# Kernel tuning notes

Measured on AMD Instinct MI355X. Metric: run time of the kernel, lower is better.

The kernel has to match this reference:

```python
import jax, jax.numpy as jnp
import numpy as np

B, S, MSL, MQL = 512, 20, 32, 16
E, H, HQ = 32, 32, 32
V, A = 10000, 1000
D = H + S  # per-object feature dim (hidden + one-hot tag) = 52
G = 256


def _lstm_last_h(x, Wih, Whh, bih, bhh):
    # x: [N, T, E]; torch LSTM gate order i,f,g,o; returns final hidden [N, H]
    n, t, _ = x.shape
    h_dim = Whh.shape[1]
    xp = jnp.einsum('nte,ge->ntg', x, Wih) + bih + bhh  # precompute input projection

    def step(carry, xt):
        h, c = carry
        gates = xt + h @ Whh.T
        i, f, g, o = jnp.split(gates, 4, axis=-1)
        c = jax.nn.sigmoid(f) * c + jax.nn.sigmoid(i) * jnp.tanh(g)
        h = jax.nn.sigmoid(o) * jnp.tanh(c)
        return (h, c), None

    init = (jnp.zeros((n, h_dim), x.dtype), jnp.zeros((n, h_dim), x.dtype))
    (h, _), _ = jax.lax.scan(step, init, xp.transpose(1, 0, 2))
    return h


def setup_inputs() -> dict:
    key = jax.random.key(0)
    ks = jax.random.split(key, 24)
    nrm = lambda k, shp, std=0.1: (jax.random.normal(k, shp) * std).astype(jnp.float32)
    inp = {
        'story': jax.random.randint(ks[0], (B, S, MSL), 0, V),
        'question': jax.random.randint(ks[1], (B, MQL), 0, V),
        'emb': nrm(ks[2], (V, E)),
        's_Wih': nrm(ks[3], (4 * H, E)),
        's_Whh': nrm(ks[4], (4 * H, H)),
        's_bih': jnp.zeros((4 * H,), jnp.float32),
        's_bhh': jnp.zeros((4 * H,), jnp.float32),
        'q_Wih': nrm(ks[5], (4 * HQ, E)),
        'q_Whh': nrm(ks[6], (4 * HQ, HQ)),
        'q_bih': jnp.zeros((4 * HQ,), jnp.float32),
        'q_bhh': jnp.zeros((4 * HQ,), jnp.float32),
        'g1_w': nrm(ks[7], (G, 2 * D + HQ)), 'g1_b': jnp.zeros((G,), jnp.float32),
        'g2_w': nrm(ks[8], (G, G)), 'g2_b': jnp.zeros((G,), jnp.float32),
        'g3_w': nrm(ks[9], (G, G)), 'g3_b': jnp.zeros((G,), jnp.float32),
        'g4_w': nrm(ks[10], (G, G)), 'g4_b': jnp.zeros((G,), jnp.float32),
        'f1_w': nrm(ks[11], (G, G)), 'f1_b': jnp.zeros((G,), jnp.float32),
        'f2_w': nrm(ks[12], (512, G)), 'f2_b': jnp.zeros((512,), jnp.float32),
        'f3_w': nrm(ks[13], (A, 512)), 'f3_b': jnp.zeros((A,), jnp.float32),
    }
    return inp


def reference(story, question, emb, s_Wih, s_Whh, s_bih, s_bhh,
              q_Wih, q_Whh, q_bih, q_bhh,
              g1_w, g1_b, g2_w, g2_b, g3_w, g3_b, g4_w, g4_b,
              f1_w, f1_b, f2_w, f2_b, f3_w, f3_b):
    bsz = story.shape[0]
    # story encoding: LSTM over each sentence, take final hidden state
    s_emb = emb[story].reshape(bsz * S, MSL, E)
    s_state = _lstm_last_h(s_emb, s_Wih, s_Whh, s_bih, s_bhh).reshape(bsz, S, H)
    # append one-hot position tags -> story objects [B, S, H+S]
    tags = jnp.broadcast_to(jnp.eye(S, dtype=s_state.dtype), (bsz, S, S))
    obj = jnp.concatenate([s_state, tags], axis=2)
    # question encoding
    q_state = _lstm_last_h(emb[question], q_Wih, q_Whh, q_bih, q_bhh)  # [B, HQ]
    # g_theta over all S*S pairs: g1(cat(o_i, o_j, q)) split into three projections
    Wa, Wb, Wq = g1_w[:, :D], g1_w[:, D:2 * D], g1_w[:, 2 * D:]
    pi = jnp.einsum('bsd,gd->bsg', obj, Wa)   # object-as-first projection
    pj = jnp.einsum('bsd,gd->bsg', obj, Wb)   # object-as-second projection
    pq = q_state @ Wq.T                        # [B, G]
    x = jax.nn.relu(pi[:, :, None, :] + pj[:, None, :, :] + pq[:, None, None, :] + g1_b)  # [B,S,S,G]
    x = jax.nn.relu(jnp.einsum('bijg,hg->bijh', x, g2_w) + g2_b)
    x = jax.nn.relu(jnp.einsum('bijg,hg->bijh', x, g3_w) + g3_b)
    x = jax.nn.relu(jnp.einsum('bijg,hg->bijh', x, g4_w) + g4_b)
    sum_g = x.sum(axis=(1, 2))  # [B, G]
    out = jax.nn.relu(sum_g @ f1_w.T + f1_b)
    out = jax.nn.relu(out @ f2_w.T + f2_b)
    return out @ f3_w.T + f3_b
```

## Files before the change

### kernel.cpp

```cpp
#include <hip/hip_runtime.h>

typedef unsigned short u16;
typedef unsigned int   u32;
typedef __attribute__((ext_vector_type(8))) short short8;
typedef __attribute__((ext_vector_type(4))) float f32x4;

#define OFF_XPS   0
#define OFF_XPQ   1280000
#define OFF_QST   2560000
#define OFF_PI    2576384
#define OFF_PJ    5197824
#define OFF_QA    7819264
#define OFF_TGA   7950336
#define OFF_TGB   7955456
#define OFF_WB    7960576
#define OFF_STB   8058880
#define OFF_WAB   8222720
#define OFF_WBB   8226816
#define OFF_WHHS  8230912
#define OFF_WHHQ  8232960
#define OFF_WF1   8235008
#define OFF_WF2   8267776
#define OFF_WF3   8333312
#define OFF_SGP   0
#define OFF_ACT1  720896
#define OFF_ACT2  786432

__device__ __forceinline__ u16 f2bf(float f){
  union { float f; u32 u; } v; v.f = f;
  u32 u = v.u;
  u32 r = u + 0x7fffu + ((u >> 16) & 1u);
  return (u16)(r >> 16);
}
__device__ __forceinline__ u32 pack2(float a, float b){
  u32 r;
  asm("v_cvt_pk_bf16_f32 %0, %1, %2" : "=v"(r) : "v"(a), "v"(b));
  return r;
}
__device__ __forceinline__ float sigm(float x){
  return __builtin_amdgcn_rcpf(1.f + __expf(-x));
}

__global__ __launch_bounds__(256) void prep_kernel(
    const float* __restrict__ emb,
    const float* __restrict__ swih, const float* __restrict__ sbih, const float* __restrict__ sbhh,
    const float* __restrict__ qwih, const float* __restrict__ qbih, const float* __restrict__ qbhh,
    const float* __restrict__ g2w, const float* __restrict__ g3w, const float* __restrict__ g4w,
    const float* __restrict__ g1w,
    const float* __restrict__ swhh, const float* __restrict__ qwhh,
    const float* __restrict__ f1w, const float* __restrict__ f2w, const float* __restrict__ f3w,
    float* __restrict__ xps, float* __restrict__ xpq,
    u16* __restrict__ wb, u16* __restrict__ wab, u16* __restrict__ wbb,
    float* __restrict__ tga, float* __restrict__ tgb,
    u16* __restrict__ whhbs, u16* __restrict__ whhbq,
    u16* __restrict__ wf1, u16* __restrict__ wf2, u16* __restrict__ wf3)
{
  __shared__ float wl[4096];
  __shared__ float bl[128];
  const int tid = threadIdx.x;
  if (blockIdx.y == 2){
    const int B = 196608;
    const int C = B + 16384;
    const int D = C + 10240;
    const int E = D + 8192;
    const int F = E + 65536;
    const int G = F + 131072;
    const int H = G + 524288;
    for (int idx = blockIdx.x*256 + tid; idx < H; idx += 40*256){
      if (idx < B){
        const int k = idx;
        const float* src = (k < 65536) ? g2w : ((k < 131072) ? g3w : g4w);
        wb[k] = f2bf(src[k & 65535]);
      } else if (idx < C){
        const int k = idx - B;
        if (k < 8192) wab[k] = f2bf(g1w[(k>>5)*136 + (k&31)]);
        else { const int k2 = k - 8192; wbb[k2] = f2bf(g1w[(k2>>5)*136 + 52 + (k2&31)]); }
      } else if (idx < D){
        const int k = idx - C;
        if (k < 5120){ const int s = k >> 8, g = k & 255; tga[k] = g1w[g*136 + 32 + s]; }
        else { const int k2 = k - 5120; const int s = k2 >> 8, g = k2 & 255; tgb[k2] = g1w[g*136 + 84 + s]; }
      } else if (idx < E){
        const int k = idx - D;
        if (k < 4096) whhbs[k] = f2bf(swhh[k]);
        else whhbq[k-4096] = f2bf(qwhh[k-4096]);
      } else if (idx < F){
        const int k = idx - E;
        wf1[k] = f2bf(f1w[k]);
      } else if (idx < G){
        const int k = idx - F;
        wf2[k] = f2bf(f2w[k]);
      } else {
        const int k = idx - G;
        const int o = k >> 9, kk = k & 511;
        wf3[k] = (o < 1000) ? f2bf(f3w[o*512 + kk]) : (u16)0;
      }
    }
    return;
  }
  const bool isq = blockIdx.y;
  const float* wih = isq ? qwih : swih;
  const float* bih = isq ? qbih : sbih;
  const float* bhh = isq ? qbhh : sbhh;
  float* xp = isq ? xpq : xps;
  #pragma unroll
  for (int k=0;k<16;k++) wl[k*256+tid] = wih[k*256+tid];
  if (tid < 128) bl[tid] = bih[tid] + bhh[tid];
  __syncthreads();
  const int v = blockIdx.x*256 + tid;
  if (v >= 10000) return;
  float4 e[8];
  #pragma unroll
  for (int q=0;q<8;q++) e[q] = *(const float4*)(emb + v*32 + q*4);
  for (int g=0; g<128; ++g){
    float acc = bl[g];
    #pragma unroll
    for (int q=0;q<8;q++){
      float4 w4 = *(const float4*)(&wl[g*32 + q*4]);
      acc = fmaf(e[q].x, w4.x, acc); acc = fmaf(e[q].y, w4.y, acc);
      acc = fmaf(e[q].z, w4.z, acc); acc = fmaf(e[q].w, w4.w, acc);
    }
    xp[v*128 + (g&15)*8 + (g>>4)] = acc;
  }
}

template<int LEN>
__device__ __forceinline__ void lstm_mfma_run(
    const int* __restrict__ toks, int s0,
    const float* __restrict__ xpr, const u16* __restrict__ whhb,
    u16* __restrict__ hl, int lane, float* h0r, float* h1r)
{
  const int l15 = lane & 15, l4 = lane >> 4;
  short8 wf[8];
  #pragma unroll
  for (int f=0; f<8; f++)
    wf[f] = *(const short8*)(whhb + (f*16+l15)*32 + l4*8);
  short8 ha = (short8){0,0,0,0,0,0,0,0};
  float c0[4] = {0,0,0,0}, c1[4] = {0,0,0,0};
  int tk[4];
  #pragma unroll
  for (int r=0;r<4;r++) tk[r] = toks[(s0 + l4*4 + r)*LEN];
  float4 xa[4], xb[4];
  #pragma unroll
  for (int r=0;r<4;r++){
    xa[r] = *(const float4*)(xpr + tk[r]*128 + l15*8);
    xb[r] = *(const float4*)(xpr + tk[r]*128 + l15*8 + 4);
  }
  #pragma unroll
  for (int t=0; t<LEN; ++t){
    int tkn[4];
    if (t+1 < LEN){
      #pragma unroll
      for (int r=0;r<4;r++) tkn[r] = toks[(s0 + l4*4 + r)*LEN + t + 1];
    }
    const f32x4 z = (f32x4){0.f,0.f,0.f,0.f};
    f32x4 acc[8];
    #pragma unroll
    for (int f=0; f<8; f++)
      acc[f] = __builtin_amdgcn_mfma_f32_16x16x32_bf16(ha, wf[f], z, 0, 0, 0);
    float4 na[4], nb[4];
    if (t+1 < LEN){
      #pragma unroll
      for (int r=0;r<4;r++){
        na[r] = *(const float4*)(xpr + tkn[r]*128 + l15*8);
        nb[r] = *(const float4*)(xpr + tkn[r]*128 + l15*8 + 4);
      }
    }
    #pragma unroll
    for (int r=0;r<4;r++){
      float i0 = sigm(acc[0][r] + xa[r].x);
      float f0 = sigm(acc[2][r] + xa[r].z);
      float g0 = 2.f*sigm(2.f*(acc[4][r] + xb[r].x)) - 1.f;
      float o0 = sigm(acc[6][r] + xb[r].z);
      c0[r] = fmaf(f0, c0[r], i0*g0);
      h0r[r] = o0 * (2.f*sigm(2.f*c0[r]) - 1.f);
      float i1 = sigm(acc[1][r] + xa[r].y);
      float f1v = sigm(acc[3][r] + xa[r].w);
      float g1v = 2.f*sigm(2.f*(acc[5][r] + xb[r].y)) - 1.f;
      float o1 = sigm(acc[7][r] + xb[r].w);
      c1[r] = fmaf(f1v, c1[r], i1*g1v);
      h1r[r] = o1 * (2.f*sigm(2.f*c1[r]) - 1.f);
    }
    if (t+1 < LEN){
      #pragma unroll
      for (int r=0;r<4;r++){
        hl[(l4*4+r)*32 + l15]      = f2bf(h0r[r]);
        hl[(l4*4+r)*32 + 16 + l15] = f2bf(h1r[r]);
      }
      __syncthreads();
      ha = *(const short8*)(hl + l15*32 + l4*8);
      #pragma unroll
      for (int r=0;r<4;r++){ xa[r] = na[r]; xb[r] = nb[r]; }
    }
  }
}

__global__ __launch_bounds__(64) void lstm_kernel(
    const int* __restrict__ story, const int* __restrict__ question,
    const float* __restrict__ xprs, const float* __restrict__ xprq,
    const u16* __restrict__ whhbs, const u16* __restrict__ whhbq,
    u16* __restrict__ stb, float* __restrict__ qst)
{
  __shared__ u16 hl[512];
  const int lane = threadIdx.x;
  const int w = blockIdx.x;
  const int l15 = lane & 15, l4 = lane >> 4;
  float h0r[4], h1r[4];
  if (w >= 640){
    const int s0 = (w - 640)*16;
    lstm_mfma_run<16>(question, s0, xprq, whhbq, hl, lane, h0r, h1r);
    #pragma unroll
    for (int r=0;r<4;r++){
      qst[(s0 + l4*4 + r)*32 + l15]      = h0r[r];
      qst[(s0 + l4*4 + r)*32 + 16 + l15] = h1r[r];
    }
  } else {
    const int s0 = w*16;
    lstm_mfma_run<32>(story, s0, xprs, whhbs, hl, lane, h0r, h1r);
    #pragma unroll
    for (int r=0;r<4;r++){
      stb[(s0 + l4*4 + r)*32 + l15]      = f2bf(h0r[r]);
      stb[(s0 + l4*4 + r)*32 + 16 + l15] = f2bf(h1r[r]);
    }
  }
}

__global__ __launch_bounds__(256) void pipj_kernel(
    const u16* __restrict__ stb, const u16* __restrict__ wab, const u16* __restrict__ wbb,
    const float* __restrict__ tga, const float* __restrict__ tgb,
    const float* __restrict__ qst, const float* __restrict__ g1w, const float* __restrict__ g1b,
    float* __restrict__ pi, float* __restrict__ pj, float* __restrict__ qa)
{
  const int tid = threadIdx.x;
  if (blockIdx.y == 2){
    for (int idx = blockIdx.x*256 + tid; idx < 131072; idx += 160*256){
      const int b = idx >> 8, g = idx & 255;
      const float* qs = qst + b*32;
      const float* wr = g1w + g*136 + 104;
      float acc = g1b[g];
      #pragma unroll
      for (int q=0;q<8;q++){
        float4 s4 = *(const float4*)(qs + q*4);
        float4 w4 = *(const float4*)(wr + q*4);
        acc = fmaf(s4.x, w4.x, acc); acc = fmaf(s4.y, w4.y, acc);
        acc = fmaf(s4.z, w4.z, acc); acc = fmaf(s4.w, w4.w, acc);
      }
      qa[idx] = acc;
    }
    return;
  }
  const int lane = tid & 63;
  const int wv = tid >> 6;
  const int l15 = lane & 15;
  const int l4r = lane >> 4;
  const int bs0 = blockIdx.x * 64;
  const bool isj = blockIdx.y;
  const u16* wB = isj ? wbb : wab;
  const float* tg = isj ? tgb : tga;
  float* out = isj ? pj : pi;

  short8 af[4], bf[4];
  #pragma unroll
  for (int mf=0; mf<4; mf++)
    af[mf] = *(const short8*)(stb + (bs0 + mf*16 + l15)*32 + l4r*8);
  #pragma unroll
  for (int nf=0; nf<4; nf++)
    bf[nf] = *(const short8*)(wB + (wv*64 + nf*16 + l15)*32 + l4r*8);

  #pragma unroll
  for (int mf=0; mf<4; mf++){
    #pragma unroll
    for (int nf=0; nf<4; nf++){
      f32x4 acc = (f32x4){0.f,0.f,0.f,0.f};
      acc = __builtin_amdgcn_mfma_f32_16x16x32_bf16(af[mf], bf[nf], acc, 0, 0, 0);
      const int g = wv*64 + nf*16 + l15;
      #pragma unroll
      for (int r=0; r<4; r++){
        const int bs = bs0 + mf*16 + l4r*4 + r;
        const int s = bs % 20;
        out[bs*256 + g] = acc[r] + tg[s*256 + g];
      }
    }
  }
}

#define LDX 264
__global__ __launch_bounds__(512) void relnet_kernel(
    const float* __restrict__ pi, const float* __restrict__ pj, const float* __restrict__ qa,
    const u16* __restrict__ w2, const u16* __restrict__ w3, const u16* __restrict__ w4,
    const float* __restrict__ b2, const float* __restrict__ b3, const float* __restrict__ b4,
    float* __restrict__ sgp)
{
  __shared__ u16 Xs[80*LDX + 6656];
  const int tid = threadIdx.x;
  const int lane = tid & 63;
  const int wv  = tid >> 6;
  const int b   = blockIdx.x;
  const int t   = blockIdx.y;
  const int l15 = lane & 15;
  const int l4  = lane >> 4;

  const float* pib = pi + b*(20*256);
  const float* pjb = pj + b*(20*256);
  const float* qab = qa + b*256;

  #pragma unroll
  for (int it = 0; it < 5; ++it){
    int u  = it*512 + tid;
    int m  = u >> 5;
    int gq = (u & 31) << 3;
    int R  = t*80 + m;
    int i  = R / 20;
    int j  = R - i*20;
    const float4* pr = (const float4*)(pib + i*256 + gq);
    const float4* qr = (const float4*)(pjb + j*256 + gq);
    const float4* ar = (const float4*)(qab + gq);
    uint4 pk;
    {
      float4 a = pr[0], c4 = qr[0], d4 = ar[0];
      pk.x = pack2(fmaxf(a.x+c4.x+d4.x,0.f), fmaxf(a.y+c4.y+d4.y,0.f));
      pk.y = pack2(fmaxf(a.z+c4.z+d4.z,0.f), fmaxf(a.w+c4.w+d4.w,0.f));
    }
    {
      float4 a = pr[1], c4 = qr[1], d4 = ar[1];
      pk.z = pack2(fmaxf(a.x+c4.x+d4.x,0.f), fmaxf(a.y+c4.y+d4.y,0.f));
      pk.w = pack2(fmaxf(a.z+c4.z+d4.z,0.f), fmaxf(a.w+c4.w+d4.w,0.f));
    }
    *(uint4*)(&Xs[m*LDX + gq]) = pk;
  }
  __syncthreads();

  for (int lay = 0; lay < 2; ++lay){
    const u16*   W    = lay ? w3 : w2;
    const float* bias = lay ? b3 : b2;
    f32x4 acc[2][5];
    #pragma unroll
    for (int hf=0; hf<2; hf++)
      #pragma unroll
      for (int mf=0; mf<5; mf++)
        acc[hf][mf] = (f32x4){0.f,0.f,0.f,0.f};

    #pragma unroll
    for (int kk = 0; kk < 8; ++kk){
      short8 af[2], xf[5];
      #pragma unroll
      for (int hf=0; hf<2; hf++){
        int row = wv*32 + hf*16 + l15;
        af[hf] = *(const short8*)(W + row*256 + kk*32 + l4*8);
      }
      #pragma unroll
      for (int mf=0; mf<5; mf++)
        xf[mf] = *(const short8*)(&Xs[(mf*16 + l15)*LDX + kk*32 + l4*8]);
      #pragma unroll
      for (int hf=0; hf<2; hf++)
        #pragma unroll
        for (int mf=0; mf<5; mf++)
          acc[hf][mf] = __builtin_amdgcn_mfma_f32_16x16x32_bf16(af[hf], xf[mf], acc[hf][mf], 0, 0, 0);
    }

    __syncthreads();
    #pragma unroll
    for (int hf=0; hf<2; hf++){
      int h0 = wv*32 + hf*16 + l4*4;
      float4 bi = *(const float4*)(bias + h0);
      #pragma unroll
      for (int mf=0; mf<5; mf++){
        int m = mf*16 + l15;
        uint2 pk;
        pk.x = pack2(fmaxf(acc[hf][mf][0]+bi.x,0.f), fmaxf(acc[hf][mf][1]+bi.y,0.f));
        pk.y = pack2(fmaxf(acc[hf][mf][2]+bi.z,0.f), fmaxf(acc[hf][mf][3]+bi.w,0.f));
        *(uint2*)(&Xs[m*LDX + h0]) = pk;
      }
    }
    __syncthreads();
  }

  {
    f32x4 acc[2][5];
    #pragma unroll
    for (int hf=0; hf<2; hf++)
      #pragma unroll
      for (int mf=0; mf<5; mf++)
        acc[hf][mf] = (f32x4){0.f,0.f,0.f,0.f};

    #pragma unroll
    for (int kk = 0; kk < 8; ++kk){
      short8 af[2], xf[5];
      #pragma unroll
      for (int hf=0; hf<2; hf++){
        int row = wv*32 + hf*16 + l15;
        af[hf] = *(const short8*)(w4 + row*256 + kk*32 + l4*8);
      }
      #pragma unroll
      for (int mf=0; mf<5; mf++)
        xf[mf] = *(const short8*)(&Xs[(mf*16 + l15)*LDX + kk*32 + l4*8]);
      #pragma unroll
      for (int hf=0; hf<2; hf++)
        #pragma unroll
        for (int mf=0; mf<5; mf++)
          acc[hf][mf] = __builtin_amdgcn_mfma_f32_16x16x32_bf16(af[hf], xf[mf], acc[hf][mf], 0, 0, 0);
    }

    #pragma unroll
    for (int hf=0; hf<2; hf++){
      int h0 = wv*32 + hf*16 + l4*4;
      float4 bi = *(const float4*)(b4 + h0);
      float s0 = 0.f, s1 = 0.f, s2 = 0.f, s3 = 0.f;
      #pragma unroll
      for (int mf=0; mf<5; mf++){
        s0 += fmaxf(acc[hf][mf][0]+bi.x,0.f);
        s1 += fmaxf(acc[hf][mf][1]+bi.y,0.f);
        s2 += fmaxf(acc[hf][mf][2]+bi.z,0.f);
        s3 += fmaxf(acc[hf][mf][3]+bi.w,0.f);
      }
      float sv[4] = {s0, s1, s2, s3};
      #pragma unroll
      for (int r=0; r<4; r++){
        float v = sv[r];
        v += __shfl_xor(v, 1);
        v += __shfl_xor(v, 2);
        v += __shfl_xor(v, 4);
        v += __shfl_xor(v, 8);
        if (l15 == 0){
          int h = h0 + r;
          sgp[t*131072 + b*256 + h] = v;
        }
      }
    }
  }
}

__global__ __launch_bounds__(256) void fcm1_kernel(
    const float* __restrict__ sgp, const u16* __restrict__ w,
    const float* __restrict__ bias, u16* __restrict__ outp)
{
  const int tid = threadIdx.x, lane = tid & 63, wv = tid >> 6;
  const int l15 = lane & 15, l4 = lane >> 4;
  const int b0 = blockIdx.x*16;
  const int of0 = blockIdx.y*4 + wv;
  f32x4 acc = (f32x4){0.f,0.f,0.f,0.f};
  #pragma unroll
  for (int kk=0; kk<8; ++kk){
    const float* base = sgp + (b0+l15)*256 + kk*32 + l4*8;
    float4 s0 = {0.f,0.f,0.f,0.f}, s1 = {0.f,0.f,0.f,0.f};
    #pragma unroll
    for (int t=0;t<5;t++){
      float4 a = *(const float4*)(base + t*131072);
      float4 c = *(const float4*)(base + t*131072 + 4);
      s0.x += a.x; s0.y += a.y; s0.z += a.z; s0.w += a.w;
      s1.x += c.x; s1.y += c.y; s1.z += c.z; s1.w += c.w;
    }
    union { short8 s; u32 u[4]; } xf;
    xf.u[0] = pack2(s0.x, s0.y); xf.u[1] = pack2(s0.z, s0.w);
    xf.u[2] = pack2(s1.x, s1.y); xf.u[3] = pack2(s1.z, s1.w);
    short8 af = *(const short8*)(w + (of0*16 + l15)*256 + kk*32 + l4*8);
    acc = __builtin_amdgcn_mfma_f32_16x16x32_bf16(af, xf.s, acc, 0, 0, 0);
  }
  const int b = b0 + l15;
  const int o0 = of0*16 + l4*4;
  float v0 = fmaxf(acc[0] + bias[o0+0], 0.f);
  float v1 = fmaxf(acc[1] + bias[o0+1], 0.f);
  float v2 = fmaxf(acc[2] + bias[o0+2], 0.f);
  float v3 = fmaxf(acc[3] + bias[o0+3], 0.f);
  uint2 pk;
  pk.x = pack2(v0, v1);
  pk.y = pack2(v2, v3);
  *(uint2*)(outp + (size_t)b*256 + o0) = pk;
}

template<int HF, int KK, int OPAD, int OREAL, int MODE>
__global__ __launch_bounds__(256) void fcm_kernel(
    const u16* __restrict__ in, const u16* __restrict__ w,
    const float* __restrict__ bias, void* __restrict__ outp)
{
  const int K = KK*32;
  const int tid = threadIdx.x, lane = tid & 63, wv = tid >> 6;
  const int l15 = lane & 15, l4 = lane >> 4;
  const int b0 = blockIdx.x*16;
  const int of0 = (blockIdx.y*4 + wv)*HF;
  f32x4 acc[HF];
  #pragma unroll
  for (int hf=0; hf<HF; hf++) acc[hf] = (f32x4){0.f,0.f,0.f,0.f};
  #pragma unroll 4
  for (int kk=0; kk<KK; ++kk){
    short8 xf = *(const short8*)(in + (b0+l15)*K + kk*32 + l4*8);
    #pragma unroll
    for (int hf=0; hf<HF; hf++){
      short8 af = *(const short8*)(w + ((of0+hf)*16 + l15)*K + kk*32 + l4*8);
      acc[hf] = __builtin_amdgcn_mfma_f32_16x16x32_bf16(af, xf, acc[hf], 0, 0, 0);
    }
  }
  const int b = b0 + l15;
  #pragma unroll
  for (int hf=0; hf<HF; hf++){
    const int o0 = (of0+hf)*16 + l4*4;
    float v[4];
    #pragma unroll
    for (int r=0;r<4;r++){
      float bv = (o0+r < OREAL) ? bias[o0+r] : 0.f;
      v[r] = acc[hf][r] + bv;
    }
    if (MODE == 0){
      uint2 pk;
      pk.x = pack2(fmaxf(v[0],0.f), fmaxf(v[1],0.f));
      pk.y = pack2(fmaxf(v[2],0.f), fmaxf(v[3],0.f));
      *(uint2*)((u16*)outp + (size_t)b*OPAD + o0) = pk;
    } else {
      float* of = (float*)outp;
      #pragma unroll
      for (int r=0;r<4;r++)
        if (o0+r < OREAL) of[(size_t)b*OREAL + o0 + r] = v[r];
    }
  }
}

extern "C" void kernel_launch(void* const* d_in, const int* in_sizes, int n_in,
                              void* d_out, int out_size, void* d_ws, size_t ws_size,
                              hipStream_t stream)
{
  const int*   story    = (const int*)d_in[0];
  const int*   question = (const int*)d_in[1];
  const float* emb   = (const float*)d_in[2];
  const float* s_wih = (const float*)d_in[3];
  const float* s_whh = (const float*)d_in[4];
  const float* s_bih = (const float*)d_in[5];
  const float* s_bhh = (const float*)d_in[6];
  const float* q_wih = (const float*)d_in[7];
  const float* q_whh = (const float*)d_in[8];
  const float* q_bih = (const float*)d_in[9];
  const float* q_bhh = (const float*)d_in[10];
  const float* g1w = (const float*)d_in[11];
  const float* g1b = (const float*)d_in[12];
  const float* g2w = (const float*)d_in[13];
  const float* g2b = (const float*)d_in[14];
  const float* g3w = (const float*)d_in[15];
  const float* g3b = (const float*)d_in[16];
  const float* g4w = (const float*)d_in[17];
  const float* g4b = (const float*)d_in[18];
  const float* f1w = (const float*)d_in[19];
  const float* f1b = (const float*)d_in[20];
  const float* f2w = (const float*)d_in[21];
  const float* f2b = (const float*)d_in[22];
  const float* f3w = (const float*)d_in[23];
  const float* f3b = (const float*)d_in[24];

  float* ws  = (float*)d_ws;
  float* xps = ws + OFF_XPS;
  float* xpq = ws + OFF_XPQ;
  float* qst = ws + OFF_QST;
  float* pi  = ws + OFF_PI;
  float* pj  = ws + OFF_PJ;
  float* qa  = ws + OFF_QA;
  float* tga = ws + OFF_TGA;
  float* tgb = ws + OFF_TGB;
  float* sgp = ws + OFF_SGP;
  u16*   wb    = (u16*)(ws + OFF_WB);
  u16*   w2b   = wb;
  u16*   w3b   = wb + 65536;
  u16*   w4b   = wb + 131072;
  u16*   stb   = (u16*)(ws + OFF_STB);
  u16*   wab   = (u16*)(ws + OFF_WAB);
  u16*   wbb   = (u16*)(ws + OFF_WBB);
  u16*   whhbs = (u16*)(ws + OFF_WHHS);
  u16*   whhbq = (u16*)(ws + OFF_WHHQ);
  u16*   wf1   = (u16*)(ws + OFF_WF1);
  u16*   wf2   = (u16*)(ws + OFF_WF2);
  u16*   wf3   = (u16*)(ws + OFF_WF3);
  u16*   act1  = (u16*)(ws + OFF_ACT1);
  u16*   act2  = (u16*)(ws + OFF_ACT2);

  prep_kernel<<<dim3(40,3), dim3(256), 0, stream>>>(
      emb, s_wih, s_bih, s_bhh, q_wih, q_bih, q_bhh,
      g2w, g3w, g4w, g1w, s_whh, q_whh, f1w, f2w, f3w,
      xps, xpq, wb, wab, wbb, tga, tgb, whhbs, whhbq, wf1, wf2, wf3);
  lstm_kernel<<<dim3(672), dim3(64), 0, stream>>>(
      story, question, xps, xpq, whhbs, whhbq, stb, qst);
  pipj_kernel<<<dim3(160,3), dim3(256), 0, stream>>>(
      stb, wab, wbb, tga, tgb, qst, g1w, g1b, pi, pj, qa);
  relnet_kernel<<<dim3(512,5), dim3(512), 0, stream>>>(
      pi, pj, qa, w2b, w3b, w4b, g2b, g3b, g4b, sgp);
  fcm1_kernel<<<dim3(32,4), dim3(256), 0, stream>>>(sgp, wf1, f1b, act1);
  fcm_kernel<2,8,512,512,0><<<dim3(32,4), dim3(256), 0, stream>>>(act1, wf2, f2b, act2);
  fcm_kernel<2,16,1024,1000,1><<<dim3(32,8), dim3(256), 0, stream>>>(act2, wf3, f3b, (float*)d_out);
}
```

Measured before the change: 244.2 us.

## Prefetch next weight fragments across layers in relnet and widen prep grid

In the relation-network MLP kernel, the weight fragments for the next k-step are loaded into registers one step ahead, including across layer boundaries (w2→w3→w4). This hides global-load latency behind the MFMAs. Plain __syncthreads are replaced with an LDS-only wait plus barrier, so outstanding global prefetches do not stall at the barrier. The prep kernel grid also grows from 40 to 160 blocks in x, with a matching stride, to spread the weight conversion work over more CUs. The cost is extra register pressure from the prefetch buffers.

```diff
diff --git a/kernel.cpp b/kernel.cpp
--- a/kernel.cpp
+++ b/kernel.cpp
@@ -41,6 +41,12 @@
   return __builtin_amdgcn_rcpf(1.f + __expf(-x));
 }
 
+#define LBAR() do {                                        \
+    asm volatile("s_waitcnt lgkmcnt(0)" ::: "memory");     \
+    __builtin_amdgcn_s_barrier();                          \
+    __builtin_amdgcn_sched_barrier(0);                     \
+  } while (0)
+
 __global__ __launch_bounds__(256) void prep_kernel(
     const float* __restrict__ emb,
     const float* __restrict__ swih, const float* __restrict__ sbih, const float* __restrict__ sbhh,
@@ -66,7 +72,7 @@
     const int F = E + 65536;
     const int G = F + 131072;
     const int H = G + 524288;
-    for (int idx = blockIdx.x*256 + tid; idx < H; idx += 40*256){
+    for (int idx = blockIdx.x*256 + tid; idx < H; idx += 160*256){
       if (idx < B){
         const int k = idx;
         const float* src = (k < 65536) ? g2w : ((k < 131072) ? g3w : g4w);
@@ -303,6 +309,9 @@
   const float* pjb = pj + b*(20*256);
   const float* qab = qa + b*256;
 
+  const int ar0 = (wv*32 + l15)*256 + l4*8;
+  const int ar1 = (wv*32 + 16 + l15)*256 + l4*8;
+
   #pragma unroll
   for (int it = 0; it < 5; ++it){
     int u  = it*512 + tid;
@@ -327,10 +336,16 @@
     }
     *(uint4*)(&Xs[m*LDX + gq]) = pk;
   }
-  __syncthreads();
-
+
+  short8 pf0 = *(const short8*)(w2 + ar0);
+  short8 pf1 = *(const short8*)(w2 + ar1);
+
+  LBAR();
+
+  #pragma unroll
   for (int lay = 0; lay < 2; ++lay){
     const u16*   W    = lay ? w3 : w2;
+    const u16*   Wn   = lay ? w4 : w3;
     const float* bias = lay ? b3 : b2;
     f32x4 acc[2][5];
     #pragma unroll
@@ -341,23 +356,23 @@
 
     #pragma unroll
     for (int kk = 0; kk < 8; ++kk){
-      short8 af[2], xf[5];
-      #pragma unroll
-      for (int hf=0; hf<2; hf++){
-        int row = wv*32 + hf*16 + l15;
-        af[hf] = *(const short8*)(W + row*256 + kk*32 + l4*8);
-      }
+      short8 a0 = pf0, a1 = pf1;
+      const u16* src = (kk < 7) ? W : Wn;
+      const int  kn  = (kk < 7) ? (kk+1)*32 : 0;
+      pf0 = *(const short8*)(src + ar0 + kn);
+      pf1 = *(const short8*)(src + ar1 + kn);
+      short8 xf[5];
       #pragma unroll
       for (int mf=0; mf<5; mf++)
         xf[mf] = *(const short8*)(&Xs[(mf*16 + l15)*LDX + kk*32 + l4*8]);
       #pragma unroll
-      for (int hf=0; hf<2; hf++)
-        #pragma unroll
-        for (int mf=0; mf<5; mf++)
-          acc[hf][mf] = __builtin_amdgcn_mfma_f32_16x16x32_bf16(af[hf], xf[mf], acc[hf][mf], 0, 0, 0);
-    }
-
-    __syncthreads();
+      for (int mf=0; mf<5; mf++){
+        acc[0][mf] = __builtin_amdgcn_mfma_f32_16x16x32_bf16(a0, xf[mf], acc[0][mf], 0, 0, 0);
+        acc[1][mf] = __builtin_amdgcn_mfma_f32_16x16x32_bf16(a1, xf[mf], acc[1][mf], 0, 0, 0);
+      }
+    }
+
+    LBAR();
     #pragma unroll
     for (int hf=0; hf<2; hf++){
       int h0 = wv*32 + hf*16 + l4*4;
@@ -371,7 +386,7 @@
         *(uint2*)(&Xs[m*LDX + h0]) = pk;
       }
     }
-    __syncthreads();
+    LBAR();
   }
 
   {
@@ -384,20 +399,20 @@
 
     #pragma unroll
     for (int kk = 0; kk < 8; ++kk){
-      short8 af[2], xf[5];
-      #pragma unroll
-      for (int hf=0; hf<2; hf++){
-        int row = wv*32 + hf*16 + l15;
-        af[hf] = *(const short8*)(w4 + row*256 + kk*32 + l4*8);
-      }
+      short8 a0 = pf0, a1 = pf1;
+      if (kk < 7){
+        pf0 = *(const short8*)(w4 + ar0 + (kk+1)*32);
+        pf1 = *(const short8*)(w4 + ar1 + (kk+1)*32);
+      }
+      short8 xf[5];
       #pragma unroll
       for (int mf=0; mf<5; mf++)
         xf[mf] = *(const short8*)(&Xs[(mf*16 + l15)*LDX + kk*32 + l4*8]);
       #pragma unroll
-      for (int hf=0; hf<2; hf++)
-        #pragma unroll
-        for (int mf=0; mf<5; mf++)
-          acc[hf][mf] = __builtin_amdgcn_mfma_f32_16x16x32_bf16(af[hf], xf[mf], acc[hf][mf], 0, 0, 0);
+      for (int mf=0; mf<5; mf++){
+        acc[0][mf] = __builtin_amdgcn_mfma_f32_16x16x32_bf16(a0, xf[mf], acc[0][mf], 0, 0, 0);
+        acc[1][mf] = __builtin_amdgcn_mfma_f32_16x16x32_bf16(a1, xf[mf], acc[1][mf], 0, 0, 0);
+      }
     }
 
     #pragma unroll
@@ -568,7 +583,7 @@
   u16*   act1  = (u16*)(ws + OFF_ACT1);
   u16*   act2  = (u16*)(ws + OFF_ACT2);
 
-  prep_kernel<<<dim3(40,3), dim3(256), 0, stream>>>(
+  prep_kernel<<<dim3(160,3), dim3(256), 0, stream>>>(
       emb, s_wih, s_bih, s_bhh, q_wih, q_bih, q_bhh,
       g2w, g3w, g4w, g1w, s_whh, q_whh, f1w, f2w, f3w,
       xps, xpq, wb, wab, wbb, tga, tgb, whhbs, whhbq, wf1, wf2, wf3);
```

After: 236.0 us. -3.3%, faster.
